# Kernel optimization log

Measured on AMD Instinct MI355X. Metric: run time of the kernel, lower is better.

The kernel has to match this reference:

```python
import jax, jax.numpy as jnp
import numpy as np

COMBS = ((0, 1), (0, 2), (1, 2))
OUT_DIM, TIME_RANK, RANK = 3, 4, 4


def grid_sample_nd(grid, coords):
    """Multilinear interpolation. grid: [C, *R] (d spatial dims), coords: [N, d] in [-1, 1].
    align_corners=True, border clamp. Returns [N, C]."""
    d = coords.shape[-1]
    i0s, ws = [], []
    for k in range(d):
        R = grid.shape[1 + k]
        x = jnp.clip((coords[:, k] + 1.0) * 0.5 * (R - 1), 0.0, R - 1)
        i0 = jnp.clip(jnp.floor(x).astype(jnp.int32), 0, R - 2)
        i0s.append(i0)
        ws.append(x - i0)
    out = jnp.zeros((grid.shape[0], coords.shape[0]), grid.dtype)
    for corner in range(2 ** d):
        idx, w = [], jnp.ones((coords.shape[0],), grid.dtype)
        for k in range(d):
            b = (corner >> k) & 1
            idx.append(i0s[k] + b)
            w = w * (ws[k] if b else 1.0 - ws[k])
        out = out + grid[(slice(None),) + tuple(idx)] * w  # [C, N]
    return out.T


def setup_inputs():
    key = jax.random.key(0)
    ks = jax.random.split(key, 16)
    n_rays, S = 4096, 128
    N = n_rays * S
    R, T, F = 128, 150, 32
    rays_d = jax.random.normal(ks[0], (n_rays, 3), jnp.float32)
    pts = jax.random.uniform(ks[1], (N, 3), jnp.float32, -1.0, 1.0)
    times = jax.random.uniform(ks[2], (N,), jnp.float32, -1.0, 1.0)
    deltas = jax.random.uniform(ks[3], (N,), jnp.float32) * 0.02 + 1e-3
    ridx = jnp.repeat(jnp.arange(n_rays, dtype=jnp.int32), S)
    boundary = (jnp.arange(N) % S) == 0
    bg_color = jax.random.uniform(ks[4], (n_rays, 3), jnp.float32)
    grid_space = jax.random.normal(ks[5], (3, RANK * OUT_DIM * TIME_RANK, R, R), jnp.float32) * 0.1
    grid_time = jax.random.normal(ks[6], (OUT_DIM * TIME_RANK, T), jnp.float32) * 0.1
    features = jax.random.normal(ks[7], (F, R, R, R), jnp.float32) * 0.1
    W1 = jax.random.normal(ks[8], (F + 3, 64), jnp.float32) * 0.05
    b1 = jnp.zeros((64,), jnp.float32)
    W2 = jax.random.normal(ks[9], (64, 16), jnp.float32) * 0.05
    b2 = jnp.zeros((16,), jnp.float32)
    Wc1 = jax.random.normal(ks[10], (15 + 3, 64), jnp.float32) * 0.05
    bc1 = jnp.zeros((64,), jnp.float32)
    Wc2 = jax.random.normal(ks[11], (64, 3), jnp.float32) * 0.05
    bc2 = jnp.zeros((3,), jnp.float32)
    return {"rays_d": rays_d, "pts": pts, "times": times, "deltas": deltas,
            "bg_color": bg_color, "grid_space": grid_space, "grid_time": grid_time,
            "features": features, "W1": W1, "b1": b1, "W2": W2, "b2": b2,
            "Wc1": Wc1, "bc1": bc1, "Wc2": Wc2, "bc2": bc2,
            "ridx": ridx, "boundary": boundary}


def reference(rays_d, pts, times, deltas, bg_color, grid_space, grid_time, features,
              W1, b1, W2, b2, Wc1, bc1, Wc2, bc2, ridx, boundary):
    n_rays = rays_d.shape[0]
    N = pts.shape[0]
    rays_d = rays_d / jnp.linalg.norm(rays_d, axis=-1, keepdims=True)
    rd = rays_d[ridx]  # [N, 3] per-sample ray dirs

    # --- low-rank spatio-temporal feature coordinates ---
    it = grid_sample_nd(grid_time, times[:, None]).reshape(N, OUT_DIM, TIME_RANK)
    sp = jnp.stack([grid_sample_nd(grid_space[c], pts[:, list(comb)])
                    for c, comb in enumerate(COMBS)])  # [3, N, rank*out*tr]
    sp = sp.reshape(3, N, OUT_DIM, TIME_RANK, RANK)
    sp = jnp.prod(sp, axis=0).sum(axis=-1)            # [N, out_dim, time_rank]
    coords = jnp.clip((sp * it).sum(axis=-1), -1.0, 1.0)  # [N, 3]
    feats = grid_sample_nd(features, coords)          # [N, F]

    # --- MLP decoder (sigma + color) ---
    h = jax.nn.relu(jnp.concatenate([feats, rd], axis=-1) @ W1 + b1)
    s = h @ W2 + b2
    sigma = jnp.exp(jnp.clip(s[:, 0], -15.0, 15.0))   # trunc_exp
    geo = s[:, 1:]
    hc = jax.nn.relu(jnp.concatenate([geo, rd], axis=-1) @ Wc1 + bc1)
    rgb = jax.nn.sigmoid(hc @ Wc2 + bc2)              # [N, 3]

    # --- segment volumetric integration (exclusive transmittance) ---
    tau = sigma * deltas
    excl = jnp.cumsum(tau) - tau
    bmask = boundary.astype(tau.dtype)
    seg_first = jax.ops.segment_sum(excl * bmask, ridx, num_segments=n_rays)
    Tr = jnp.exp(-(excl - seg_first[ridx]))
    w = Tr * (1.0 - jnp.exp(-tau))                    # per-sample weights
    ray_colors = jax.ops.segment_sum(w[:, None] * rgb, ridx, num_segments=n_rays)
    alpha = jax.ops.segment_sum(w, ridx, num_segments=n_rays)
    return ray_colors + (1.0 - alpha)[:, None] * bg_color
```

## Files before the change

kernel.cpp:

```cpp
#include <hip/hip_runtime.h>
#include <hip/hip_fp16.h>
#include <math.h>

#define RR 128
#define TT 150
#define NCH 48
#define NF 32

typedef float vf2 __attribute__((ext_vector_type(2)));
typedef unsigned int u4v __attribute__((ext_vector_type(4)));
typedef _Float16 h2 __attribute__((ext_vector_type(2)));

__device__ __forceinline__ void up4(uint u, float s, float* a) {
    vf2 lo = __builtin_amdgcn_cvt_pk_f32_fp8(u, false);
    vf2 hi = __builtin_amdgcn_cvt_pk_f32_fp8(u, true);
    a[0] = fmaf(s, lo[0], a[0]); a[1] = fmaf(s, lo[1], a[1]);
    a[2] = fmaf(s, hi[0], a[2]); a[3] = fmaf(s, hi[1], a[3]);
}
__device__ __forceinline__ void up16(u4v q, float s, float* a) {
    up4(q[0], s, a + 0); up4(q[1], s, a + 4);
    up4(q[2], s, a + 8); up4(q[3], s, a + 12);
}
__device__ __forceinline__ float dot2(h2 a, h2 b, float c) {
    return __builtin_amdgcn_fdot2(a, b, c, false);
}
__device__ __forceinline__ h2 pack2(float a, float b) {
    h2 r; r[0] = (_Float16)a; r[1] = (_Float16)b; return r;
}
__device__ __forceinline__ h2 ash2(uint u) { return __builtin_bit_cast(h2, u); }

__global__ __launch_bounds__(256) void tgsp_8(const float* __restrict__ in,
                                              uint* __restrict__ out) {
    __shared__ float lds[48][65];
    const int t = threadIdx.x;
    const int p = blockIdx.x >> 8;
    const int tile = blockIdx.x & 255;
    const size_t V = (size_t)RR * RR;
    const size_t v0 = (size_t)tile * 64;
    const float* ip = in + (size_t)p * NCH * V;
    uint* op = out + (size_t)p * V * 12;
    #pragma unroll
    for (int k = 0; k < 12; k++) {
        int idx = k * 256 + t; int c = idx >> 6; int vv = idx & 63;
        lds[c][vv] = ip[(size_t)c * V + v0 + vv];
    }
    __syncthreads();
    #pragma unroll
    for (int k = 0; k < 3; k++) {
        int idx = k * 256 + t; int vv = idx / 12; int cp = idx - vv * 12;
        float a = lds[4 * cp + 0][vv] * 128.f;
        float b = lds[4 * cp + 1][vv] * 128.f;
        float c = lds[4 * cp + 2][vv] * 128.f;
        float d = lds[4 * cp + 3][vv] * 128.f;
        uint w = (uint)__builtin_amdgcn_cvt_pk_fp8_f32(a, b, 0, false);
        w = (uint)__builtin_amdgcn_cvt_pk_fp8_f32(c, d, w, true);
        op[(v0 + vv) * 12 + cp] = w;
    }
}

template<bool TR>
__global__ __launch_bounds__(256, 5) void lrv_main(
    const float* __restrict__ rays_d,
    const float* __restrict__ pts,
    const float* __restrict__ times,
    const float* __restrict__ deltas,
    const float* __restrict__ bg,
    const void* __restrict__ gspace_p,
    const float* __restrict__ gtime,
    const float* __restrict__ feat,
    const float* __restrict__ W1, const float* __restrict__ b1,
    const float* __restrict__ W2, const float* __restrict__ b2,
    const float* __restrict__ Wc1, const float* __restrict__ bc1,
    const float* __restrict__ Wc2, const float* __restrict__ bc2,
    const int*  __restrict__ ridx,
    float* __restrict__ out)
{
    __shared__ __align__(16) h2 sW1d[18 * 64];
    __shared__ __align__(16) h2 sW2d[32 * 16];
    __shared__ __align__(16) h2 sWc1d[9 * 64];
    __shared__ __align__(16) h2 sWc2d[32 * 3];
    __shared__ float sb1[64], sbc1[64], sb2[16], sbc2[4];
    __shared__ __align__(16) float4 sFeatV[8][8];
    __shared__ int sV[4], sU[4];
    __shared__ float waveTot[4];
    __shared__ float4 rbuf[4];

    const int tid  = threadIdx.x;
    const int lane = tid & 63;
    const int wv   = tid >> 6;

    {
        for (int k = tid; k < 18 * 64; k += 256) {
            int ip = k >> 6, j = k & 63;
            int i1 = 2 * ip + 1;
            float w0 = W1[(2 * ip) * 64 + j];
            float w1 = (i1 < 35) ? W1[i1 * 64 + j] : 0.f;
            sW1d[k] = pack2(w0, w1);
        }
        for (int k = tid; k < 32 * 16; k += 256) {
            int jp = k >> 4, kk = k & 15;
            sW2d[k] = pack2(W2[(2 * jp) * 16 + kk], W2[(2 * jp + 1) * 16 + kk]);
        }
        for (int k = tid; k < 9 * 64; k += 256) {
            int ip = k >> 6, j = k & 63;
            sWc1d[k] = pack2(Wc1[(2 * ip) * 64 + j], Wc1[(2 * ip + 1) * 64 + j]);
        }
        for (int k = tid; k < 32 * 3; k += 256) {
            int jp = k / 3, c = k - jp * 3;
            sWc2d[k] = pack2(Wc2[(2 * jp) * 3 + c], Wc2[(2 * jp + 1) * 3 + c]);
        }
        if (tid < 64) { sb1[tid] = b1[tid]; sbc1[tid] = bc1[tid]; }
        if (tid < 16) sb2[tid] = b2[tid];
        if (tid < 3)  sbc2[tid] = bc2[tid];
    }
    __syncthreads();

    const int ray = blockIdx.x * 2 + (tid >> 7);
    const int i   = ray * 128 + (tid & 127);

    float itv[12];
    {
        float t = times[i];
        float x = (t + 1.f) * 0.5f * (float)(TT - 1);
        x = fminf(fmaxf(x, 0.f), (float)(TT - 1));
        int ti0 = (int)floorf(x);
        ti0 = min(max(ti0, 0), TT - 2);
        float tw = x - (float)ti0;
        #pragma unroll
        for (int c = 0; c < 12; c++) {
            float v0 = gtime[c * TT + ti0];
            float v1 = gtime[c * TT + ti0 + 1];
            itv[c] = fmaf(tw, v1 - v0, v0);
        }
    }

    float p0 = pts[i * 3 + 0], p1 = pts[i * 3 + 1], p2 = pts[i * 3 + 2];
    int   pbia[3], pbib[3];
    float pw[3][4];
    {
        const float pa[3] = { p0, p0, p1 };
        const float pb[3] = { p1, p2, p2 };
        #pragma unroll
        for (int c = 0; c < 3; c++) {
            float xa = fminf(fmaxf((pa[c] + 1.f) * 0.5f * (float)(RR - 1), 0.f), (float)(RR - 1));
            float xb = fminf(fmaxf((pb[c] + 1.f) * 0.5f * (float)(RR - 1), 0.f), (float)(RR - 1));
            int ia = min(max((int)floorf(xa), 0), RR - 2);
            int ib = min(max((int)floorf(xb), 0), RR - 2);
            float wa = xa - (float)ia, wb = xb - (float)ib;
            pbia[c] = ia; pbib[c] = ib;
            pw[c][0] = (1.f - wa) * (1.f - wb);
            pw[c][1] = (1.f - wa) * wb;
            pw[c][2] = wa * (1.f - wb);
            pw[c][3] = wa * wb;
        }
    }
    float S12[12];
    if constexpr (TR) {
        const uint* gs = (const uint*)gspace_p;
        uint b[3][4];
        #pragma unroll
        for (int c = 0; c < 3; c++) {
            uint b00 = ((uint)c * (RR * RR) + (uint)pbia[c] * RR + (uint)pbib[c]) * 12u;
            b[c][0] = b00;            b[c][1] = b00 + 12u;
            b[c][2] = b00 + RR * 12u; b[c][3] = b00 + RR * 12u + 12u;
        }
        #pragma unroll
        for (int cb = 0; cb < 3; cb++) {
            float pr[16];
            #pragma unroll
            for (int p = 0; p < 3; p++) {
                float a[16];
                #pragma unroll
                for (int j = 0; j < 16; j++) a[j] = 0.f;
                #pragma unroll
                for (int corner = 0; corner < 4; corner++) {
                    u4v q = *reinterpret_cast<const u4v*>(gs + b[p][corner] + cb * 4);
                    up16(q, pw[p][corner] * 0.0078125f, a);
                }
                #pragma unroll
                for (int j = 0; j < 16; j++) pr[j] = (p == 0) ? a[j] : pr[j] * a[j];
            }
            #pragma unroll
            for (int g = 0; g < 4; g++)
                S12[cb * 4 + g] = pr[g * 4 + 0] + pr[g * 4 + 1]
                                + pr[g * 4 + 2] + pr[g * 4 + 3];
        }
    } else {
        const float* gs = (const float*)gspace_p;
        #pragma unroll
        for (int k = 0; k < 12; k++) S12[k] = 0.f;
        #pragma unroll 4
        for (int ch = 0; ch < NCH; ch++) {
            float prod = 1.f;
            #pragma unroll
            for (int c = 0; c < 3; c++) {
                const float* g = gs + (size_t)(c * NCH + ch) * (RR * RR)
                               + pbia[c] * RR + pbib[c];
                float v = pw[c][0] * g[0] + pw[c][1] * g[1]
                        + pw[c][2] * g[RR] + pw[c][3] * g[RR + 1];
                prod *= v;
            }
            S12[ch >> 2] += prod;
        }
    }
    float cc[3];
    #pragma unroll
    for (int o = 0; o < 3; o++) {
        float a = 0.f;
        #pragma unroll
        for (int t = 0; t < 4; t++) a += S12[o * 4 + t] * itv[o * 4 + t];
        cc[o] = fminf(fmaxf(a, -1.f), 1.f);
    }

    __align__(16) float in35[36];
    int   fi[3];
    float cw[8];
    {
        float fw[3];
        #pragma unroll
        for (int k = 0; k < 3; k++) {
            float xk = fminf(fmaxf((cc[k] + 1.f) * 0.5f * (float)(RR - 1), 0.f), (float)(RR - 1));
            int ik = min(max((int)floorf(xk), 0), RR - 2);
            fi[k] = ik; fw[k] = xk - (float)ik;
        }
        float w0 = fw[0], w1 = fw[1], w2 = fw[2];
        cw[0] = (1.f - w0) * (1.f - w1) * (1.f - w2);
        cw[1] = (1.f - w0) * (1.f - w1) * w2;
        cw[2] = (1.f - w0) * w1 * (1.f - w2);
        cw[3] = (1.f - w0) * w1 * w2;
        cw[4] = w0 * (1.f - w1) * (1.f - w2);
        cw[5] = w0 * (1.f - w1) * w2;
        cw[6] = w0 * w1 * (1.f - w2);
        cw[7] = w0 * w1 * w2;
    }
    {
        int packed = (fi[0] << 16) | (fi[1] << 8) | fi[2];
        int first  = __builtin_amdgcn_readfirstlane(packed);
        unsigned long long bal = __ballot(packed == first);
        if (lane == 0) { sV[wv] = first; sU[wv] = (bal == ~0ull) ? 1 : 0; }
    }
    __syncthreads();
    const bool uni = sU[0] && sU[1] && sU[2] && sU[3] &&
                     sV[0] == sV[1] && sV[1] == sV[2] && sV[2] == sV[3];
    const size_t V3 = (size_t)RR * RR * RR;
    if (uni) {
        {
            int c  = tid >> 5;
            int ch = tid & 31;
            size_t off = (((size_t)(fi[0] + ((c >> 2) & 1)) * RR
                         + (size_t)(fi[1] + ((c >> 1) & 1))) * RR
                         + (size_t)(fi[2] + (c & 1)));
            ((float*)sFeatV)[c * 32 + ch] = feat[(size_t)ch * V3 + off];
        }
        __syncthreads();
        float4* in4 = reinterpret_cast<float4*>(in35);
        #pragma unroll
        for (int chq = 0; chq < 8; chq++) {
            float4 acc = make_float4(0.f, 0.f, 0.f, 0.f);
            #pragma unroll
            for (int c = 0; c < 8; c++) {
                float4 v = sFeatV[c][chq];
                acc.x = fmaf(cw[c], v.x, acc.x);
                acc.y = fmaf(cw[c], v.y, acc.y);
                acc.z = fmaf(cw[c], v.z, acc.z);
                acc.w = fmaf(cw[c], v.w, acc.w);
            }
            in4[chq] = acc;
        }
    } else {
        size_t fb = ((size_t)fi[0] * RR + fi[1]) * RR + fi[2];
        #pragma unroll 4
        for (int ch = 0; ch < NF; ch++) {
            const float* f = feat + (size_t)ch * V3 + fb;
            in35[ch] = cw[0] * f[0]            + cw[1] * f[1]
                     + cw[2] * f[RR]           + cw[3] * f[RR + 1]
                     + cw[4] * f[RR * RR]      + cw[5] * f[RR * RR + 1]
                     + cw[6] * f[RR * RR + RR] + cw[7] * f[RR * RR + RR + 1];
        }
    }
    {
        int r = ridx[i];
        float d0 = rays_d[r * 3 + 0], d1 = rays_d[r * 3 + 1], d2 = rays_d[r * 3 + 2];
        float inv = 1.f / sqrtf(d0 * d0 + d1 * d1 + d2 * d2);
        in35[32] = d0 * inv; in35[33] = d1 * inv; in35[34] = d2 * inv;
    }

    h2 x1[18];
    #pragma unroll
    for (int p = 0; p < 17; p++) x1[p] = pack2(in35[2 * p], in35[2 * p + 1]);
    x1[17] = pack2(in35[34], 0.f);

    float sacc[16];
    #pragma unroll
    for (int k = 0; k < 16; k++) sacc[k] = sb2[k];
    #pragma unroll 2
    for (int jb = 0; jb < 16; jb++) {
        float a0 = sb1[jb * 4 + 0], a1 = sb1[jb * 4 + 1];
        float a2 = sb1[jb * 4 + 2], a3 = sb1[jb * 4 + 3];
        #pragma unroll
        for (int p = 0; p < 18; p++) {
            u4v u = *reinterpret_cast<const u4v*>(&sW1d[p * 64 + jb * 4]);
            h2 xp = x1[p];
            a0 = dot2(xp, ash2(u[0]), a0);
            a1 = dot2(xp, ash2(u[1]), a1);
            a2 = dot2(xp, ash2(u[2]), a2);
            a3 = dot2(xp, ash2(u[3]), a3);
        }
        a0 = fmaxf(a0, 0.f); a1 = fmaxf(a1, 0.f);
        a2 = fmaxf(a2, 0.f); a3 = fmaxf(a3, 0.f);
        h2 h01 = pack2(a0, a1), h23 = pack2(a2, a3);
        #pragma unroll
        for (int q = 0; q < 4; q++) {
            u4v u0 = *reinterpret_cast<const u4v*>(&sW2d[(2 * jb) * 16 + q * 4]);
            u4v u1 = *reinterpret_cast<const u4v*>(&sW2d[(2 * jb + 1) * 16 + q * 4]);
            #pragma unroll
            for (int m = 0; m < 4; m++)
                sacc[q * 4 + m] = dot2(h01, ash2(u0[m]),
                                  dot2(h23, ash2(u1[m]), sacc[q * 4 + m]));
        }
    }
    float sigma = expf(fminf(fmaxf(sacc[0], -15.f), 15.f));

    h2 xc[9];
    #pragma unroll
    for (int p = 0; p < 7; p++) xc[p] = pack2(sacc[2 * p + 1], sacc[2 * p + 2]);
    xc[7] = pack2(sacc[15], in35[32]);
    xc[8] = pack2(in35[33], in35[34]);

    float rc0 = sbc2[0], rc1 = sbc2[1], rc2 = sbc2[2];
    #pragma unroll 2
    for (int jb = 0; jb < 16; jb++) {
        float a0 = sbc1[jb * 4 + 0], a1 = sbc1[jb * 4 + 1];
        float a2 = sbc1[jb * 4 + 2], a3 = sbc1[jb * 4 + 3];
        #pragma unroll
        for (int p = 0; p < 9; p++) {
            u4v u = *reinterpret_cast<const u4v*>(&sWc1d[p * 64 + jb * 4]);
            h2 xp = xc[p];
            a0 = dot2(xp, ash2(u[0]), a0);
            a1 = dot2(xp, ash2(u[1]), a1);
            a2 = dot2(xp, ash2(u[2]), a2);
            a3 = dot2(xp, ash2(u[3]), a3);
        }
        a0 = fmaxf(a0, 0.f); a1 = fmaxf(a1, 0.f);
        a2 = fmaxf(a2, 0.f); a3 = fmaxf(a3, 0.f);
        h2 h01 = pack2(a0, a1), h23 = pack2(a2, a3);
        int jp0 = 2 * jb, jp1 = 2 * jb + 1;
        rc0 = dot2(h01, sWc2d[jp0 * 3 + 0], dot2(h23, sWc2d[jp1 * 3 + 0], rc0));
        rc1 = dot2(h01, sWc2d[jp0 * 3 + 1], dot2(h23, sWc2d[jp1 * 3 + 1], rc1));
        rc2 = dot2(h01, sWc2d[jp0 * 3 + 2], dot2(h23, sWc2d[jp1 * 3 + 2], rc2));
    }
    float r_ = 1.f / (1.f + expf(-rc0));
    float g_ = 1.f / (1.f + expf(-rc1));
    float b_ = 1.f / (1.f + expf(-rc2));

    float tau = sigma * deltas[i];
    float v = tau;
    #pragma unroll
    for (int off = 1; off < 64; off <<= 1) {
        float u = __shfl_up(v, off, 64);
        if (lane >= off) v += u;
    }
    if (lane == 63) waveTot[wv] = v;
    float excl = v - tau;
    __syncthreads();
    if (wv & 1) excl += waveTot[wv & 2];

    float Tr = expf(-excl);
    float w  = Tr * (1.f - expf(-tau));

    float ax = w * r_, ay = w * g_, az = w * b_, aw = w;
    #pragma unroll
    for (int off = 32; off; off >>= 1) {
        ax += __shfl_down(ax, off, 64);
        ay += __shfl_down(ay, off, 64);
        az += __shfl_down(az, off, 64);
        aw += __shfl_down(aw, off, 64);
    }
    if (lane == 0) rbuf[wv] = make_float4(ax, ay, az, aw);
    __syncthreads();
    if (lane == 0 && (wv & 1) == 0) {
        float cx = rbuf[wv].x + rbuf[wv + 1].x;
        float cy = rbuf[wv].y + rbuf[wv + 1].y;
        float cz = rbuf[wv].z + rbuf[wv + 1].z;
        float alpha = rbuf[wv].w + rbuf[wv + 1].w;
        out[ray * 3 + 0] = cx + (1.f - alpha) * bg[ray * 3 + 0];
        out[ray * 3 + 1] = cy + (1.f - alpha) * bg[ray * 3 + 1];
        out[ray * 3 + 2] = cz + (1.f - alpha) * bg[ray * 3 + 2];
    }
}

extern "C" void kernel_launch(void* const* d_in, const int* in_sizes, int n_in,
                              void* d_out, int out_size, void* d_ws, size_t ws_size,
                              hipStream_t stream) {
    const float* rays_d = (const float*)d_in[0];
    const float* pts    = (const float*)d_in[1];
    const float* times  = (const float*)d_in[2];
    const float* deltas = (const float*)d_in[3];
    const float* bg     = (const float*)d_in[4];
    const float* gspace = (const float*)d_in[5];
    const float* gtime  = (const float*)d_in[6];
    const float* feat   = (const float*)d_in[7];
    const float* W1  = (const float*)d_in[8];
    const float* b1  = (const float*)d_in[9];
    const float* W2  = (const float*)d_in[10];
    const float* b2  = (const float*)d_in[11];
    const float* Wc1 = (const float*)d_in[12];
    const float* bc1 = (const float*)d_in[13];
    const float* Wc2 = (const float*)d_in[14];
    const float* bc2 = (const float*)d_in[15];
    const int*   ridx = (const int*)d_in[16];

    const int n_rays = in_sizes[0] / 3;

    const size_t GSP_8B = (size_t)3 * RR * RR * NCH;

    if (ws_size >= GSP_8B) {
        uint* gsp_t = (uint*)d_ws;
        tgsp_8<<<dim3(3 * 256), dim3(256), 0, stream>>>(gspace, gsp_t);
        lrv_main<true><<<dim3(n_rays / 2), dim3(256), 0, stream>>>(
            rays_d, pts, times, deltas, bg, (const void*)gsp_t, gtime, feat,
            W1, b1, W2, b2, Wc1, bc1, Wc2, bc2, ridx, (float*)d_out);
    } else {
        lrv_main<false><<<dim3(n_rays / 2), dim3(256), 0, stream>>>(
            rays_d, pts, times, deltas, bg, (const void*)gspace, gtime, feat,
            W1, b1, W2, b2, Wc1, bc1, Wc2, bc2, ridx, (float*)d_out);
    }
}
```

Measured before the change: 143.9 us.

## Run the sigma MLP layers on MFMA via per-wave LDS staging

Replaces the per-thread packed-dot2 evaluation of the first decoder layer (35→64) and the second layer (64→16) with 16x16x16 f16 MFMA instructions. Each wave writes its 64 input vectors into a new LDS tile, multiplies them against transposed fp16 weights, and writes the 16 outputs back to LDS, reusing the same buffer for each lane to read back. This is meant to remove the large count of scalar dot2 instructions and per-thread weight loads from LDS. In exchange it adds about 24 KB of LDS per block and an extra LDS round trip, and lowers the launch-bounds occupancy hint from 5 to 4.

```diff
diff --git a/kernel.cpp b/kernel.cpp
--- a/kernel.cpp
+++ b/kernel.cpp
@@ -10,6 +10,8 @@
 typedef float vf2 __attribute__((ext_vector_type(2)));
 typedef unsigned int u4v __attribute__((ext_vector_type(4)));
 typedef _Float16 h2 __attribute__((ext_vector_type(2)));
+typedef _Float16 h4 __attribute__((ext_vector_type(4)));
+typedef float fv4 __attribute__((ext_vector_type(4)));
 
 __device__ __forceinline__ void up4(uint u, float s, float* a) {
     vf2 lo = __builtin_amdgcn_cvt_pk_f32_fp8(u, false);
@@ -59,7 +61,7 @@
 }
 
 template<bool TR>
-__global__ __launch_bounds__(256, 5) void lrv_main(
+__global__ __launch_bounds__(256, 4) void lrv_main(
     const float* __restrict__ rays_d,
     const float* __restrict__ pts,
     const float* __restrict__ times,
@@ -75,8 +77,9 @@
     const int*  __restrict__ ridx,
     float* __restrict__ out)
 {
-    __shared__ __align__(16) h2 sW1d[18 * 64];
-    __shared__ __align__(16) h2 sW2d[32 * 16];
+    __shared__ __align__(16) _Float16 sW1t[64 * 48];
+    __shared__ __align__(16) _Float16 sW2t[16 * 72];
+    __shared__ __align__(16) _Float16 sX[4 * 64 * 48];
     __shared__ __align__(16) h2 sWc1d[9 * 64];
     __shared__ __align__(16) h2 sWc2d[32 * 3];
     __shared__ float sb1[64], sbc1[64], sb2[16], sbc2[4];
@@ -88,18 +91,17 @@
     const int tid  = threadIdx.x;
     const int lane = tid & 63;
     const int wv   = tid >> 6;
-
-    {
-        for (int k = tid; k < 18 * 64; k += 256) {
-            int ip = k >> 6, j = k & 63;
-            int i1 = 2 * ip + 1;
-            float w0 = W1[(2 * ip) * 64 + j];
-            float w1 = (i1 < 35) ? W1[i1 * 64 + j] : 0.f;
-            sW1d[k] = pack2(w0, w1);
-        }
-        for (int k = tid; k < 32 * 16; k += 256) {
-            int jp = k >> 4, kk = k & 15;
-            sW2d[k] = pack2(W2[(2 * jp) * 16 + kk], W2[(2 * jp + 1) * 16 + kk]);
+    const int lg   = lane >> 4;
+    const int ll   = lane & 15;
+
+    {
+        for (int k = tid; k < 64 * 48; k += 256) {
+            int n = k / 48, kk = k - n * 48;
+            sW1t[k] = (_Float16)((kk < 35) ? W1[kk * 64 + n] : 0.f);
+        }
+        for (int k = tid; k < 16 * 64; k += 256) {
+            int o = k >> 6, n = k & 63;
+            sW2t[o * 72 + n] = (_Float16)W2[n * 16 + o];
         }
         for (int k = tid; k < 9 * 64; k += 256) {
             int ip = k >> 6, j = k & 63;
@@ -285,39 +287,80 @@
         in35[32] = d0 * inv; in35[33] = d1 * inv; in35[34] = d2 * inv;
     }
 
-    h2 x1[18];
-    #pragma unroll
-    for (int p = 0; p < 17; p++) x1[p] = pack2(in35[2 * p], in35[2 * p + 1]);
-    x1[17] = pack2(in35[34], 0.f);
+    _Float16* Xw = sX + wv * (64 * 48);
+    float* Srow  = (float*)Xw;
+
+    {
+        u4v xw[6];
+        #pragma unroll
+        for (int t6 = 0; t6 < 6; t6++) {
+            #pragma unroll
+            for (int e = 0; e < 4; e++) {
+                int q = t6 * 4 + e;
+                float a = (2 * q     < 35) ? in35[2 * q]     : 0.f;
+                float b = (2 * q + 1 < 35) ? in35[2 * q + 1] : 0.f;
+                xw[t6][e] = __builtin_bit_cast(uint, pack2(a, b));
+            }
+        }
+        u4v* xrow = (u4v*)(Xw + lane * 48);
+        #pragma unroll
+        for (int t6 = 0; t6 < 6; t6++) xrow[t6] = xw[t6];
+    }
+
+    fv4 bb[4];
+    #pragma unroll
+    for (int hr = 0; hr < 4; hr++)
+        bb[hr] = *(const fv4*)&sb1[hr * 16 + (lg << 2)];
+    fv4 b2v = *(const fv4*)&sb2[lg << 2];
+
+    #pragma unroll
+    for (int half = 0; half < 2; half++) {
+        fv4 acc1[4][2];
+        #pragma unroll
+        for (int hr = 0; hr < 4; hr++) {
+            acc1[hr][0] = bb[hr];
+            acc1[hr][1] = bb[hr];
+        }
+        #pragma unroll
+        for (int ks = 0; ks < 3; ks++) {
+            h4 a1[4], b1f[2];
+            #pragma unroll
+            for (int hr = 0; hr < 4; hr++)
+                a1[hr] = *(const h4*)&sW1t[(hr * 16 + ll) * 48 + ks * 16 + (lg << 2)];
+            #pragma unroll
+            for (int s2 = 0; s2 < 2; s2++) {
+                int sc = half * 2 + s2;
+                b1f[s2] = *(const h4*)&Xw[(sc * 16 + ll) * 48 + ks * 16 + (lg << 2)];
+            }
+            #pragma unroll
+            for (int hr = 0; hr < 4; hr++) {
+                acc1[hr][0] = __builtin_amdgcn_mfma_f32_16x16x16f16(a1[hr], b1f[0], acc1[hr][0], 0, 0, 0);
+                acc1[hr][1] = __builtin_amdgcn_mfma_f32_16x16x16f16(a1[hr], b1f[1], acc1[hr][1], 0, 0, 0);
+            }
+        }
+        #pragma unroll
+        for (int s2 = 0; s2 < 2; s2++) {
+            fv4 acc2 = b2v;
+            #pragma unroll
+            for (int ks = 0; ks < 4; ks++) {
+                fv4 g = acc1[ks][s2];
+                h4 hb;
+                #pragma unroll
+                for (int e = 0; e < 4; e++) hb[e] = (_Float16)fmaxf(g[e], 0.f);
+                h4 a2 = *(const h4*)&sW2t[ll * 72 + ks * 16 + (lg << 2)];
+                acc2 = __builtin_amdgcn_mfma_f32_16x16x16f16(a2, hb, acc2, 0, 0, 0);
+            }
+            int sc = half * 2 + s2;
+            *(fv4*)&Srow[(sc * 16 + ll) * 20 + (lg << 2)] = acc2;
+        }
+    }
 
     float sacc[16];
     #pragma unroll
-    for (int k = 0; k < 16; k++) sacc[k] = sb2[k];
-    #pragma unroll 2
-    for (int jb = 0; jb < 16; jb++) {
-        float a0 = sb1[jb * 4 + 0], a1 = sb1[jb * 4 + 1];
-        float a2 = sb1[jb * 4 + 2], a3 = sb1[jb * 4 + 3];
-        #pragma unroll
-        for (int p = 0; p < 18; p++) {
-            u4v u = *reinterpret_cast<const u4v*>(&sW1d[p * 64 + jb * 4]);
-            h2 xp = x1[p];
-            a0 = dot2(xp, ash2(u[0]), a0);
-            a1 = dot2(xp, ash2(u[1]), a1);
-            a2 = dot2(xp, ash2(u[2]), a2);
-            a3 = dot2(xp, ash2(u[3]), a3);
-        }
-        a0 = fmaxf(a0, 0.f); a1 = fmaxf(a1, 0.f);
-        a2 = fmaxf(a2, 0.f); a3 = fmaxf(a3, 0.f);
-        h2 h01 = pack2(a0, a1), h23 = pack2(a2, a3);
-        #pragma unroll
-        for (int q = 0; q < 4; q++) {
-            u4v u0 = *reinterpret_cast<const u4v*>(&sW2d[(2 * jb) * 16 + q * 4]);
-            u4v u1 = *reinterpret_cast<const u4v*>(&sW2d[(2 * jb + 1) * 16 + q * 4]);
-            #pragma unroll
-            for (int m = 0; m < 4; m++)
-                sacc[q * 4 + m] = dot2(h01, ash2(u0[m]),
-                                  dot2(h23, ash2(u1[m]), sacc[q * 4 + m]));
-        }
+    for (int q = 0; q < 4; q++) {
+        fv4 v = *(const fv4*)&Srow[lane * 20 + q * 4];
+        sacc[q * 4 + 0] = v[0]; sacc[q * 4 + 1] = v[1];
+        sacc[q * 4 + 2] = v[2]; sacc[q * 4 + 3] = v[3];
     }
     float sigma = expf(fminf(fmaxf(sacc[0], -15.f), 15.f));
 
```

Measured after the change: 119.1 us. 1.21x faster.
